# Performance work log

Hardware: AMD Instinct MI355X
Metric: run time of the kernel (lower is better)

## Reference

```python
import jax, jax.numpy as jnp
import numpy as np

INDIM = 128
OUTDIM = 256
GRID = 16


def setup_inputs() -> dict:
    key = jax.random.key(0)
    kx, kc = jax.random.split(key)
    x = jax.random.normal(kx, (32768, INDIM), dtype=jnp.float32)
    # fouriercoeffs: (2, outdim, indim, gridsize), init randn / (sqrt(indim)*sqrt(gridsize))
    fouriercoeffs = jax.random.normal(kc, (2, OUTDIM, INDIM, GRID), dtype=jnp.float32) / (
        np.sqrt(INDIM) * np.sqrt(GRID)
    )
    bias = jnp.zeros((1, OUTDIM), dtype=jnp.float32)
    return {"x": x, "fouriercoeffs": fouriercoeffs, "bias": bias}


def reference(x, fouriercoeffs, bias):
    orig_shape = x.shape
    x2 = x.reshape(-1, INDIM)  # (N, indim)
    k = jnp.arange(1, GRID + 1, dtype=x2.dtype)  # (gridsize,)
    x_scaled = x2[:, :, None] * k  # (N, indim, gridsize)
    y = (
        jnp.einsum("nig,oig->no", jnp.cos(x_scaled), fouriercoeffs[0])
        + jnp.einsum("nig,oig->no", jnp.sin(x_scaled), fouriercoeffs[1])
        + bias
    )
    return y.reshape(*orig_shape[:-1], OUTDIM)
```

## Files before the change

### kernel.cpp

```cpp
#include <hip/hip_runtime.h>
#include <cstdint>

#define IN_DIM   128
#define OUT_DIM  256
#define NROWS    32768
#define BM       64
#define NSTEPS   32
#define STR      65

typedef unsigned short u16;
typedef __attribute__((ext_vector_type(8)))  __bf16 bf16x8;
typedef __attribute__((ext_vector_type(16))) float  f32x16;

__global__ __launch_bounds__(256) void kan_prep(const float* __restrict__ C,
                                                u16* __restrict__ Bpack) {
    const int o = threadIdx.x;
    const int i = blockIdx.x;
    const int t = blockIdx.y;
    const float* src = C + (((size_t)(t * OUT_DIM + o) * IN_DIM + i) * 16);
    bf16x8 lo = {}, hi = {};
#pragma unroll
    for (int g = 0; g < 8; ++g) {
        lo[g] = (__bf16)src[g];
        hi[g] = (__bf16)src[8 + g];
    }
    const int ko = i * 4 + t * 2;
    bf16x8* dst = (bf16x8*)Bpack;
    dst[(size_t)ko * OUT_DIM + o]       = lo;
    dst[(size_t)(ko + 1) * OUT_DIM + o] = hi;
}

__global__ __launch_bounds__(256, 2) void kan_gemm(const float* __restrict__ x,
                                                   const u16* __restrict__ Bpack,
                                                   const float* __restrict__ bias,
                                                   float* __restrict__ out) {
    __shared__ __align__(16) u16 Asm[2][16 * STR * 8];

    const int tid  = threadIdx.x;
    const int lane = tid & 63;
    const int wn   = tid >> 6;
    const int la31 = lane & 31;
    const int gh   = lane >> 5;
    const int m0   = blockIdx.x * BM;

    const int tr  = tid >> 2;
    const int til = tid & 3;

    f32x16 vz;
#pragma unroll
    for (int r = 0; r < 16; ++r) vz[r] = 0.f;
    f32x16 acc[2][2] = {{vz, vz}, {vz, vz}};

    const bf16x8* Bv = (const bf16x8*)Bpack;
    bf16x8* Av0 = (bf16x8*)Asm[0];
    bf16x8* Av1 = (bf16x8*)Asm[1];

    const float* xrow = x + (size_t)(m0 + tr) * IN_DIM + til;
    const int bcol = wn * 64 + la31;

    auto gen = [&](bf16x8* Av, float xv) {
        float s1, c1;
        __sincosf(xv, &s1, &c1);
        const float t2 = 2.f * c1;
        bf16x8 qc0 = {}, qc1 = {}, qs0 = {}, qs1 = {};
        float cp = c1, sp = s1;
        float cc = t2 * c1 - 1.f, sc = t2 * s1;
        qc0[0] = (__bf16)cp;  qs0[0] = (__bf16)sp;
        qc0[1] = (__bf16)cc;  qs0[1] = (__bf16)sc;
#pragma unroll
        for (int g = 3; g <= 16; ++g) {
            const float cn = t2 * cc - cp;
            const float sn = t2 * sc - sp;
            cp = cc; sp = sc; cc = cn; sc = sn;
            const int idx = g - 1;
            if (idx < 8) { qc0[idx] = (__bf16)cc;      qs0[idx] = (__bf16)sc; }
            else         { qc1[idx - 8] = (__bf16)cc;  qs1[idx - 8] = (__bf16)sc; }
        }
        const int kob = til * 4;
        Av[(kob + 0) * STR + tr] = qc0;
        Av[(kob + 1) * STR + tr] = qc1;
        Av[(kob + 2) * STR + tr] = qs0;
        Av[(kob + 3) * STR + tr] = qs1;
    };

    bf16x8 Bcur[8][2], Bnxt[8][2];

#pragma unroll
    for (int kw = 0; kw < 8; ++kw)
#pragma unroll
        for (int fn = 0; fn < 2; ++fn)
            Bcur[kw][fn] = Bv[(size_t)((kw >> 1) * 4 + (kw & 1) * 2 + gh) * OUT_DIM
                              + bcol + fn * 32];
    float xn = xrow[4];
    gen(Av0, xrow[0]);
    __syncthreads();

    for (int kt = 0; kt < NSTEPS; ++kt) {
        bf16x8* Avc = (kt & 1) ? Av1 : Av0;
        bf16x8* Avn = (kt & 1) ? Av0 : Av1;

        const int ktn = (kt + 1) & (NSTEPS - 1);
#pragma unroll
        for (int kw = 0; kw < 8; ++kw)
#pragma unroll
            for (int fn = 0; fn < 2; ++fn)
                Bnxt[kw][fn] = Bv[(size_t)(ktn * 16 + (kw >> 1) * 4 + (kw & 1) * 2 + gh)
                                  * OUT_DIM + bcol + fn * 32];

        if (kt + 1 < NSTEPS) {
            gen(Avn, xn);
            xn = xrow[((kt + 2) & (NSTEPS - 1)) * 4];
        }

#pragma unroll
        for (int kw = 0; kw < 8; ++kw) {
            const int koL = (kw >> 1) * 4 + (kw & 1) * 2 + gh;
            bf16x8 af[2];
#pragma unroll
            for (int fm = 0; fm < 2; ++fm)
                af[fm] = Avc[koL * STR + fm * 32 + la31];
#pragma unroll
            for (int fm = 0; fm < 2; ++fm)
#pragma unroll
                for (int fn = 0; fn < 2; ++fn)
                    acc[fm][fn] = __builtin_amdgcn_mfma_f32_32x32x16_bf16(
                        af[fm], Bcur[kw][fn], acc[fm][fn], 0, 0, 0);
        }
#pragma unroll
        for (int kw = 0; kw < 8; ++kw)
#pragma unroll
            for (int fn = 0; fn < 2; ++fn)
                Bcur[kw][fn] = Bnxt[kw][fn];
        __syncthreads();
    }

#pragma unroll
    for (int fn = 0; fn < 2; ++fn) {
        const int col = bcol + fn * 32;
        const float bv = bias[col];
#pragma unroll
        for (int fm = 0; fm < 2; ++fm) {
            const int rbase = m0 + fm * 32 + 4 * gh;
#pragma unroll
            for (int r = 0; r < 16; ++r) {
                const int row = rbase + (r & 3) + 8 * (r >> 2);
                out[(size_t)row * OUT_DIM + col] = acc[fm][fn][r] + bv;
            }
        }
    }
}

extern "C" void kernel_launch(void* const* d_in, const int* in_sizes, int n_in,
                              void* d_out, int out_size, void* d_ws, size_t ws_size,
                              hipStream_t stream) {
    const float* x    = (const float*)d_in[0];
    const float* fc   = (const float*)d_in[1];
    const float* bias = (const float*)d_in[2];
    float* out        = (float*)d_out;
    u16* Bpack        = (u16*)d_ws;

    kan_prep<<<dim3(IN_DIM, 2), OUT_DIM, 0, stream>>>(fc, Bpack);
    kan_gemm<<<dim3(NROWS / BM), 256, 0, stream>>>(x, Bpack, bias, out);
}
```

Baseline: 79.42 us.

## Generate A fragments in registers per wave, drop LDS staging and block sync

Replaces the 256-thread block, which staged the sin/cos basis in LDS with double buffering and __syncthreads, with single-wave blocks. Each wave computes its own bf16 cos/sin fragments directly in registers and covers a 64x128 output tile. This removes LDS traffic and barriers. In exchange the basis is computed twice, once for each column half, and B fragments are loaded with no prefetch across steps. Doubling the tile width also raises accumulator register pressure.

Result: slower. 95.63 us (+20.4%).

```diff
diff --git a/kernel.cpp b/kernel.cpp
--- a/kernel.cpp
+++ b/kernel.cpp
@@ -4,13 +4,12 @@
 #define IN_DIM   128
 #define OUT_DIM  256
 #define NROWS    32768
-#define BM       64
 #define NSTEPS   32
-#define STR      65
 
 typedef unsigned short u16;
 typedef __attribute__((ext_vector_type(8)))  __bf16 bf16x8;
 typedef __attribute__((ext_vector_type(16))) float  f32x16;
+typedef __attribute__((ext_vector_type(4)))  float  f32x4v;
 
 __global__ __launch_bounds__(256) void kan_prep(const float* __restrict__ C,
                                                 u16* __restrict__ Bpack) {
@@ -30,35 +29,29 @@
     dst[(size_t)(ko + 1) * OUT_DIM + o] = hi;
 }
 
-__global__ __launch_bounds__(256, 2) void kan_gemm(const float* __restrict__ x,
-                                                   const u16* __restrict__ Bpack,
-                                                   const float* __restrict__ bias,
-                                                   float* __restrict__ out) {
-    __shared__ __align__(16) u16 Asm[2][16 * STR * 8];
-
-    const int tid  = threadIdx.x;
-    const int lane = tid & 63;
-    const int wn   = tid >> 6;
+__global__ __launch_bounds__(64, 1) void kan_gemm(const float* __restrict__ x,
+                                                  const u16* __restrict__ Bpack,
+                                                  const float* __restrict__ bias,
+                                                  float* __restrict__ out) {
+    const int lane = threadIdx.x;
     const int la31 = lane & 31;
     const int gh   = lane >> 5;
-    const int m0   = blockIdx.x * BM;
-
-    const int tr  = tid >> 2;
-    const int til = tid & 3;
+    const int bid  = blockIdx.x;
+    const int wn   = bid & 1;
+    const int m0   = (bid >> 1) * 64;
 
     f32x16 vz;
 #pragma unroll
     for (int r = 0; r < 16; ++r) vz[r] = 0.f;
-    f32x16 acc[2][2] = {{vz, vz}, {vz, vz}};
+    f32x16 acc[2][4] = {{vz, vz, vz, vz}, {vz, vz, vz, vz}};
 
     const bf16x8* Bv = (const bf16x8*)Bpack;
-    bf16x8* Av0 = (bf16x8*)Asm[0];
-    bf16x8* Av1 = (bf16x8*)Asm[1];
+    const int bcol = wn * 128 + la31;
 
-    const float* xrow = x + (size_t)(m0 + tr) * IN_DIM + til;
-    const int bcol = wn * 64 + la31;
+    const float* xr0 = x + (size_t)(m0 + la31) * IN_DIM;
+    const float* xr1 = xr0 + (size_t)32 * IN_DIM;
 
-    auto gen = [&](bf16x8* Av, float xv) {
+    auto chain = [&](float xv, bf16x8& afc, bf16x8& afs) {
         float s1, c1;
         __sincosf(xv, &s1, &c1);
         const float t2 = 2.f * c1;
@@ -76,66 +69,49 @@
             if (idx < 8) { qc0[idx] = (__bf16)cc;      qs0[idx] = (__bf16)sc; }
             else         { qc1[idx - 8] = (__bf16)cc;  qs1[idx - 8] = (__bf16)sc; }
         }
-        const int kob = til * 4;
-        Av[(kob + 0) * STR + tr] = qc0;
-        Av[(kob + 1) * STR + tr] = qc1;
-        Av[(kob + 2) * STR + tr] = qs0;
-        Av[(kob + 3) * STR + tr] = qs1;
+        afc = gh ? qc1 : qc0;
+        afs = gh ? qs1 : qs0;
     };
 
-    bf16x8 Bcur[8][2], Bnxt[8][2];
+    f32x4v xa = *(const f32x4v*)(xr0);
+    f32x4v xb = *(const f32x4v*)(xr1);
+
+    for (int kt = 0; kt < NSTEPS; ++kt) {
+        const int ktn = (kt + 1) & (NSTEPS - 1);
+        const f32x4v xa_n = *(const f32x4v*)(xr0 + ktn * 4);
+        const f32x4v xb_n = *(const f32x4v*)(xr1 + ktn * 4);
 
 #pragma unroll
-    for (int kw = 0; kw < 8; ++kw)
+        for (int i = 0; i < 4; ++i) {
+            const size_t koc = (size_t)((kt * 4 + i) * 4 + gh);
+            bf16x8 bgc[4], bgs[4];
 #pragma unroll
-        for (int fn = 0; fn < 2; ++fn)
-            Bcur[kw][fn] = Bv[(size_t)((kw >> 1) * 4 + (kw & 1) * 2 + gh) * OUT_DIM
-                              + bcol + fn * 32];
-    float xn = xrow[4];
-    gen(Av0, xrow[0]);
-    __syncthreads();
+            for (int fn = 0; fn < 4; ++fn) {
+                bgc[fn] = Bv[koc * OUT_DIM + bcol + fn * 32];
+                bgs[fn] = Bv[(koc + 2) * OUT_DIM + bcol + fn * 32];
+            }
 
-    for (int kt = 0; kt < NSTEPS; ++kt) {
-        bf16x8* Avc = (kt & 1) ? Av1 : Av0;
-        bf16x8* Avn = (kt & 1) ? Av0 : Av1;
-
-        const int ktn = (kt + 1) & (NSTEPS - 1);
-#pragma unroll
-        for (int kw = 0; kw < 8; ++kw)
-#pragma unroll
-            for (int fn = 0; fn < 2; ++fn)
-                Bnxt[kw][fn] = Bv[(size_t)(ktn * 16 + (kw >> 1) * 4 + (kw & 1) * 2 + gh)
-                                  * OUT_DIM + bcol + fn * 32];
-
-        if (kt + 1 < NSTEPS) {
-            gen(Avn, xn);
-            xn = xrow[((kt + 2) & (NSTEPS - 1)) * 4];
-        }
+            bf16x8 afc0, afs0, afc1, afs1;
+            chain(xa[i], afc0, afs0);
+            chain(xb[i], afc1, afs1);
 
 #pragma unroll
-        for (int kw = 0; kw < 8; ++kw) {
-            const int koL = (kw >> 1) * 4 + (kw & 1) * 2 + gh;
-            bf16x8 af[2];
+            for (int fn = 0; fn < 4; ++fn) {
+                acc[0][fn] = __builtin_amdgcn_mfma_f32_32x32x16_bf16(afc0, bgc[fn], acc[0][fn], 0, 0, 0);
+                acc[1][fn] = __builtin_amdgcn_mfma_f32_32x32x16_bf16(afc1, bgc[fn], acc[1][fn], 0, 0, 0);
+            }
 #pragma unroll
-            for (int fm = 0; fm < 2; ++fm)
-                af[fm] = Avc[koL * STR + fm * 32 + la31];
-#pragma unroll
-            for (int fm = 0; fm < 2; ++fm)
-#pragma unroll
-                for (int fn = 0; fn < 2; ++fn)
-                    acc[fm][fn] = __builtin_amdgcn_mfma_f32_32x32x16_bf16(
-                        af[fm], Bcur[kw][fn], acc[fm][fn], 0, 0, 0);
+            for (int fn = 0; fn < 4; ++fn) {
+                acc[0][fn] = __builtin_amdgcn_mfma_f32_32x32x16_bf16(afs0, bgs[fn], acc[0][fn], 0, 0, 0);
+                acc[1][fn] = __builtin_amdgcn_mfma_f32_32x32x16_bf16(afs1, bgs[fn], acc[1][fn], 0, 0, 0);
+            }
         }
-#pragma unroll
-        for (int kw = 0; kw < 8; ++kw)
-#pragma unroll
-            for (int fn = 0; fn < 2; ++fn)
-                Bcur[kw][fn] = Bnxt[kw][fn];
-        __syncthreads();
+        xa = xa_n;
+        xb = xb_n;
     }
 
 #pragma unroll
-    for (int fn = 0; fn < 2; ++fn) {
+    for (int fn = 0; fn < 4; ++fn) {
         const int col = bcol + fn * 32;
         const float bv = bias[col];
 #pragma unroll
@@ -160,5 +136,5 @@
     u16* Bpack        = (u16*)d_ws;
 
     kan_prep<<<dim3(IN_DIM, 2), OUT_DIM, 0, stream>>>(fc, Bpack);
-    kan_gemm<<<dim3(NROWS / BM), 256, 0, stream>>>(x, Bpack, bias, out);
+    kan_gemm<<<dim3(NROWS / 64 * 2), 64, 0, stream>>>(x, Bpack, bias, out);
 }
```
